# Kernel optimization log

Measured on AMD Instinct MI355X. Metric: run time of the kernel, lower is better.

## Reference

```python
import jax, jax.numpy as jnp
import numpy as np
from jax import lax

D = 32          # link_state_dim == path_state_dim
MAX_LEN = 16    # max path length (fixed for jit)
T_ITER = 8      # message-passing iterations


def gru_cell(x, h, kernel, rec_kernel, bias):
    """Keras GRUCell, reset_after=True. bias: [2, 3H] (input bias, recurrent bias)."""
    xw = x @ kernel + bias[0]
    hw = h @ rec_kernel + bias[1]
    xz, xr, xh = jnp.split(xw, 3, axis=-1)
    hz, hr, hh = jnp.split(hw, 3, axis=-1)
    z = jax.nn.sigmoid(xz + hz)
    r = jax.nn.sigmoid(xr + hr)
    c = jnp.tanh(xh + r * hh)
    return z * h + (1.0 - z) * c


def setup_inputs() -> dict:
    n_paths, n_links = 100000, 10000
    lengths = (np.arange(n_paths) % MAX_LEN) + 1            # 1..16, avg 8.5
    E = int(lengths.sum())                                   # 850000
    path_ids = np.repeat(np.arange(n_paths), lengths).astype(np.int32)
    offsets = np.repeat(np.cumsum(lengths) - lengths, lengths)
    sequence_path = (np.arange(E) - offsets).astype(np.int32)  # 0..len-1 per path
    rng = np.random.default_rng(0)
    link_to_path = rng.integers(0, n_links, E).astype(np.int32)

    key = jax.random.key(0)
    ks = jax.random.split(key, 16)
    p = {
        'capacity': jax.random.uniform(ks[0], (n_links, 1), jnp.float32) + 0.1,
        'traffic': jax.random.uniform(ks[1], (n_paths, 1), jnp.float32),
        'packets': jax.random.uniform(ks[2], (n_paths, 1), jnp.float32),
        'time_dist_params': jax.random.normal(ks[3], (n_paths, 12), jnp.float32),
        'path_kernel': 0.2 * jax.random.normal(ks[4], (D, 3 * D), jnp.float32),
        'path_rec_kernel': 0.2 * jax.random.normal(ks[5], (D, 3 * D), jnp.float32),
        'path_bias': jnp.zeros((2, 3 * D), jnp.float32),
        'link_kernel': 0.2 * jax.random.normal(ks[6], (D, 3 * D), jnp.float32),
        'link_rec_kernel': 0.2 * jax.random.normal(ks[7], (D, 3 * D), jnp.float32),
        'link_bias': jnp.zeros((2, 3 * D), jnp.float32),
        'w1': 0.1 * jax.random.normal(ks[8], (D, 256), jnp.float32),
        'b1': jnp.zeros((256,), jnp.float32),
        'w2': 0.1 * jax.random.normal(ks[9], (256, 256), jnp.float32),
        'b2': jnp.zeros((256,), jnp.float32),
        'w3': 0.1 * jax.random.normal(ks[10], (256, 1), jnp.float32),
        'b3': jnp.zeros((1,), jnp.float32),
        'link_to_path': jnp.asarray(link_to_path),
        'path_ids': jnp.asarray(path_ids),
        'sequence_path': jnp.asarray(sequence_path),
        'path_to_link': jnp.asarray(path_ids),      # path index of each (link,path) incidence
        'sequence_links': jnp.asarray(link_to_path),  # link index (segment id) of each incidence
        'n_links': n_links,
        'n_paths': n_paths,
    }
    return p


def reference(capacity, traffic, packets, time_dist_params,
              path_kernel, path_rec_kernel, path_bias,
              link_kernel, link_rec_kernel, link_bias,
              w1, b1, w2, b2, w3, b3,
              link_to_path, path_ids, sequence_path, path_to_link, sequence_links,
              n_links, n_paths):
    # initial states
    link_state = jnp.concatenate([capacity, jnp.zeros((n_links, D - 1), capacity.dtype)], axis=1)
    path_state = jnp.concatenate(
        [traffic, packets, time_dist_params, jnp.zeros((n_paths, D - 14), traffic.dtype)], axis=1)

    def mp_iter(carry, _):
        link_state, path_state = carry
        # gather link states along each path, scatter into padded [P, T, D]
        link_gather = link_state[link_to_path]
        link_inputs = jnp.zeros((n_paths, MAX_LEN, D), link_state.dtype)
        link_inputs = link_inputs.at[path_ids, sequence_path].set(link_gather)
        xs = jnp.moveaxis(link_inputs, 1, 0)              # [T, P, D]
        mask = jnp.any(xs != 0.0, axis=-1)                # keras Masking semantics

        def rnn_step(h, xm):
            x, m = xm
            h_new = gru_cell(x, h, path_kernel, path_rec_kernel, path_bias)
            return jnp.where(m[:, None], h_new, h), None

        path_state, _ = lax.scan(rnn_step, path_state, (xs, mask))
        # aggregate path states back onto links
        path_gather = path_state[path_to_link]
        path_sum = jax.ops.segment_sum(path_gather, sequence_links, num_segments=n_links)
        link_state = gru_cell(path_sum, link_state, link_kernel, link_rec_kernel, link_bias)
        return (link_state, path_state), None

    (link_state, path_state), _ = lax.scan(mp_iter, (link_state, path_state), None, length=T_ITER)

    h = jax.nn.relu(path_state @ w1 + b1)
    h = jax.nn.relu(h @ w2 + b2)
    return h @ w3 + b3
```

## Files before the change

### kernel.cpp

```cpp
#include <hip/hip_runtime.h>
#include <hip/hip_bf16.h>

#define DD 32
#define GG 96

typedef __attribute__((ext_vector_type(8))) short bf16x8;
typedef __attribute__((ext_vector_type(4))) float f32x4;

__device__ __forceinline__ float frcp(float x){ return __builtin_amdgcn_rcpf(x); }
__device__ __forceinline__ float fsig(float x){
    float e = __expf(-x);
    return frcp(1.0f + e);
}
__device__ __forceinline__ float ftanh(float x){
    float ax = fabsf(x);
    float e  = __expf(-2.0f * ax);
    float t  = (1.0f - e) * frcp(1.0f + e);
    return copysignf(t, x);
}
__device__ __forceinline__ short f2bf(float f){
    union { float f; unsigned u; } v; v.f = f;
    unsigned r = v.u + 0x7fffu + ((v.u >> 16) & 1u);
    return (short)(r >> 16);
}
__device__ __forceinline__ float bf2f(short s){
    union { unsigned u; float f; } v; v.u = ((unsigned)(unsigned short)s) << 16;
    return v.f;
}
__device__ __forceinline__ void split2(float x, short& hi, short& lo){
    hi = f2bf(x);
    lo = f2bf(x - bf2f(hi));
}
__device__ __forceinline__ f32x4 splat4(float x){ f32x4 v = { x, x, x, x }; return v; }

#define MFMA3(acc, ah, al, bh, bl) do { \
    acc = __builtin_amdgcn_mfma_f32_16x16x32_bf16(ah, bh, acc, 0, 0, 0); \
    acc = __builtin_amdgcn_mfma_f32_16x16x32_bf16(al, bh, acc, 0, 0, 0); \
    acc = __builtin_amdgcn_mfma_f32_16x16x32_bf16(ah, bl, acc, 0, 0, 0); \
} while (0)


__global__ void zero_ints_kernel(int* a, int n){
    int i = blockIdx.x * blockDim.x + threadIdx.x;
    if (i < n) a[i] = 0;
}

__global__ void init_states_kernel(const float* __restrict__ cap,
                                   const float* __restrict__ traffic, const float* __restrict__ packets,
                                   const float* __restrict__ tdp,
                                   float* __restrict__ ls, short* __restrict__ lsbh, short* __restrict__ lsbl,
                                   float* __restrict__ ps, int n_links, int n_paths){
    int i = blockIdx.x * blockDim.x + threadIdx.x;
    int nl = n_links * DD;
    if (i < nl){
        int l = i >> 5, d = i & 31;
        float v = (d == 0) ? cap[l] : 0.0f;
        ls[i] = v;
        short hi, lo; split2(v, hi, lo);
        lsbh[i] = hi; lsbl[i] = lo;
        return;
    }
    int j = i - nl;
    if (j >= n_paths * DD) return;
    int p = j >> 5, d = j & 31;
    float v = 0.0f;
    if (d == 0) v = traffic[p];
    else if (d == 1) v = packets[p];
    else if (d < 14) v = tdp[p * 12 + (d - 2)];
    ps[j] = v;
}

__global__ void meta_kernel(const int* __restrict__ path_ids, const int* __restrict__ seqp,
                            const int* __restrict__ seql, int* __restrict__ start,
                            int* __restrict__ lenp, int* __restrict__ lcount, int E){
    int e = blockIdx.x * blockDim.x + threadIdx.x;
    if (e >= E) return;
    int p = path_ids[e];
    int s = seqp[e];
    if (s == 0) start[p] = e;
    if (e == E - 1 || path_ids[e + 1] != p) lenp[p] = s + 1;
    atomicAdd(&lcount[seql[e]], 1);
}

__global__ void bhist_block_kernel(const int* __restrict__ lenp, int* __restrict__ bcnt,
                                   int* __restrict__ bh, int n_paths){
    __shared__ int h[16];
    if (threadIdx.x < 16) h[threadIdx.x] = 0;
    __syncthreads();
    int p = blockIdx.x * 256 + threadIdx.x;
    if (p < n_paths) atomicAdd(&h[lenp[p] - 1], 1);
    __syncthreads();
    if (threadIdx.x < 16){
        bh[blockIdx.x * 16 + threadIdx.x] = h[threadIdx.x];
        atomicAdd(&bcnt[threadIdx.x], h[threadIdx.x]);
    }
}

__global__ void bscan2_kernel(const int* __restrict__ bcnt, const int* __restrict__ bh,
                              int* __restrict__ bb, int nblk){
    __shared__ int base[16];
    if (threadIdx.x == 0){
        int run = 0;
        for (int i = 0; i < 16; i++){ base[i] = run; run += bcnt[i]; }
    }
    __syncthreads();
    int i = threadIdx.x;
    if (i < 16){
        int run = base[i];
        for (int blk = 0; blk < nblk; ++blk){
            bb[blk * 16 + i] = run;
            run += bh[blk * 16 + i];
        }
    }
}

__global__ void bscatter2_kernel(const int* __restrict__ lenp, const int* __restrict__ bb,
                                 int* __restrict__ order, int n_paths){
    __shared__ int h[16];
    if (threadIdx.x < 16) h[threadIdx.x] = 0;
    __syncthreads();
    int p = blockIdx.x * 256 + threadIdx.x;
    if (p < n_paths){
        int b = lenp[p] - 1;
        int r = atomicAdd(&h[b], 1);
        order[bb[blockIdx.x * 16 + b] + r] = p;
    }
}

__global__ __launch_bounds__(1024) void scan_kernel(const int* __restrict__ cnt, int* __restrict__ off, int n){
    __shared__ int psh[1025];
    int tid = threadIdx.x;
    int chunk = (n + 1023) / 1024;
    int b = tid * chunk, e = min(b + chunk, n);
    int s = 0;
    for (int i = b; i < e; ++i) s += cnt[i];
    psh[tid + 1] = s;
    if (tid == 0) psh[0] = 0;
    __syncthreads();
    for (int ofs = 1; ofs < 1024; ofs <<= 1){
        int v = (tid + 1 >= ofs) ? psh[tid + 1 - ofs] : 0;
        __syncthreads();
        psh[tid + 1] += v;
        __syncthreads();
    }
    int run = psh[tid];
    for (int i = b; i < e; ++i){ off[i] = run; run += cnt[i]; }
    if (b < n && e == n) off[n] = run;
}

__global__ void fillpbl_kernel(const int* __restrict__ seql, const int* __restrict__ p2l,
                               const int* __restrict__ loff, int* __restrict__ lfill,
                               int* __restrict__ pbl, int E){
    int e = blockIdx.x * blockDim.x + threadIdx.x;
    if (e >= E) return;
    int l = seql[e];
    int pos = loff[l] + atomicAdd(&lfill[l], 1);
    pbl[pos] = p2l[e];
}

__global__ void pack_all_kernel(const float* __restrict__ pK, const float* __restrict__ pRK,
                                const float* __restrict__ lK, const float* __restrict__ lRK,
                                const float* __restrict__ w1, const float* __restrict__ w2,
                                short* __restrict__ gth, short* __restrict__ gtl,
                                short* __restrict__ rth, short* __restrict__ rtl){
    int t0 = blockIdx.x * blockDim.x + threadIdx.x;
    if (t0 < 4 * 6 * 64){
        int t = t0;
        int lane = t & 63;
        int jt = (t >> 6) % 6;
        int mat = t / (6 * 64);
        const float* W = (mat == 0) ? pK : (mat == 1) ? pRK : (mat == 2) ? lK : lRK;
        int n = lane & 15, g = lane >> 4;
        for (int i = 0; i < 8; i++){
            float w = W[(g * 8 + i) * GG + jt * 16 + n];
            short hi, lo; split2(w, hi, lo);
            gth[(size_t)t * 8 + i] = hi;
            gtl[(size_t)t * 8 + i] = lo;
        }
        return;
    }
    int t = t0 - 4 * 6 * 64;
    if (t >= 144 * 64) return;
    int lane = t & 63;
    int f = t >> 6;
    int n = lane & 15, g = lane >> 4;
    for (int i = 0; i < 8; i++){
        float w;
        if (f < 16) w = w1[(g * 8 + i) * 256 + f * 16 + n];
        else {
            int ff = f - 16, kc = ff >> 4, jt = ff & 15;
            w = w2[(kc * 32 + g * 8 + i) * 256 + jt * 16 + n];
        }
        short hi, lo; split2(w, hi, lo);
        rth[(size_t)t * 8 + i] = hi;
        rtl[(size_t)t * 8 + i] = lo;
    }
}

template<bool MASK>
__device__ __forceinline__ void gru_gates(const f32x4 accZR[4], const f32x4 accXC[2], const f32x4 accHC[2],
                                          float hD[2][4], const int lenD[4], int t)
{
    #pragma unroll
    for (int tt = 0; tt < 2; tt++){
        #pragma unroll
        for (int r = 0; r < 4; r++){
            float z = fsig(accZR[tt][r]);
            float rr = fsig(accZR[2 + tt][r]);
            float c = ftanh(accXC[tt][r] + rr * accHC[tt][r]);
            float hn = z * hD[tt][r] + (1.0f - z) * c;
            if (MASK) hD[tt][r] = (t < lenD[r]) ? hn : hD[tt][r];
            else      hD[tt][r] = hn;
        }
    }
}

__global__ __launch_bounds__(256, 1) void path_gru_kernel(
    const short* __restrict__ lsbh, const short* __restrict__ lsbl, float* __restrict__ ps,
    const int* __restrict__ l2p, const int* __restrict__ start,
    const int* __restrict__ lenp, const int* __restrict__ order,
    const short* __restrict__ gth, const short* __restrict__ gtl,
    const float* __restrict__ bias, int n_paths, int n_waves, int stride)
{
    __shared__ __align__(16) float hlds[4][16 * 36];

    int tid = threadIdx.x;
    int warp = tid >> 6;
    int lane = tid & 63;
    int l15 = lane & 15, g = lane >> 4;

    int gw = blockIdx.x * 4 + warp;
    int nw = gridDim.x * 4;
    float* hl = hlds[warp];

    bf16x8 wKh[6], wKl[6], wRKh[6], wRKl[6];
    #pragma unroll
    for (int jt = 0; jt < 6; jt++){
        wKh[jt]  = *(const bf16x8*)(gth + ((size_t)((0 * 6 + jt) * 64 + lane)) * 8);
        wKl[jt]  = *(const bf16x8*)(gtl + ((size_t)((0 * 6 + jt) * 64 + lane)) * 8);
        wRKh[jt] = *(const bf16x8*)(gth + ((size_t)((1 * 6 + jt) * 64 + lane)) * 8);
        wRKl[jt] = *(const bf16x8*)(gtl + ((size_t)((1 * 6 + jt) * 64 + lane)) * 8);
    }
    float bzr[4], bx2[2], bh2[2];
    #pragma unroll
    for (int jt = 0; jt < 4; jt++) bzr[jt] = bias[jt * 16 + l15] + bias[GG + jt * 16 + l15];
    #pragma unroll
    for (int u = 0; u < 2; u++){
        bx2[u] = bias[(4 + u) * 16 + l15];
        bh2[u] = bias[GG + (4 + u) * 16 + l15];
    }

    for (int w = gw; w < n_waves; w += nw){
        long long wp = ((long long)w * stride) % n_waves;
        int base16 = (int)wp * 16;

        int aidx = base16 + l15;
        int pa = order[min(aidx, n_paths - 1)];
        int s0 = start[pa];
        int la_c = lenp[pa];
        int la = (aidx < n_paths) ? la_c : 0;
        int maxlen = __shfl(la_c, 15);

        int pD[4], lenD[4]; bool vD[4];
        #pragma unroll
        for (int r = 0; r < 4; r++){
            int di = base16 + g * 4 + r;
            vD[r] = (di < n_paths);
            pD[r] = order[min(di, n_paths - 1)];
            lenD[r] = vD[r] ? lenp[pD[r]] : 0;
        }

        float hD[2][4];
        #pragma unroll
        for (int tt = 0; tt < 2; tt++)
            #pragma unroll
            for (int r = 0; r < 4; r++)
                hD[tt][r] = ps[(size_t)pD[r] * DD + l15 + tt * 16];

        bf16x8 hfh, hfl;
        {
            const float* hp = ps + (size_t)pa * DD + g * 8;
            #pragma unroll
            for (int i = 0; i < 8; i++){ short hi, lo; split2(hp[i], hi, lo); hfh[i] = hi; hfl[i] = lo; }
        }

        bf16x8 xfh, xfl;
        {
            int lk = l2p[s0];
            xfh = *reinterpret_cast<const bf16x8*>(lsbh + (size_t)lk * DD + g * 8);
            xfl = *reinterpret_cast<const bf16x8*>(lsbl + (size_t)lk * DD + g * 8);
        }

        for (int t = 0; t < maxlen; ++t){
            bf16x8 nxh, nxl;
            int tn = t + 1;
            if (tn < maxlen){
                int e = s0 + max(min(tn, la - 1), 0);
                int lk = l2p[e];
                nxh = *reinterpret_cast<const bf16x8*>(lsbh + (size_t)lk * DD + g * 8);
                nxl = *reinterpret_cast<const bf16x8*>(lsbl + (size_t)lk * DD + g * 8);
            }

            f32x4 accZR[4], accXC[2], accHC[2];
            #pragma unroll
            for (int jt = 0; jt < 4; jt++){
                f32x4 a = splat4(bzr[jt]);
                MFMA3(a, xfh, xfl, wKh[jt],  wKl[jt]);
                MFMA3(a, hfh, hfl, wRKh[jt], wRKl[jt]);
                accZR[jt] = a;
            }
            #pragma unroll
            for (int u = 0; u < 2; u++){
                f32x4 ax = splat4(bx2[u]);
                MFMA3(ax, xfh, xfl, wKh[4 + u], wKl[4 + u]);
                accXC[u] = ax;
                f32x4 ah = splat4(bh2[u]);
                MFMA3(ah, hfh, hfl, wRKh[4 + u], wRKl[4 + u]);
                accHC[u] = ah;
            }

            gru_gates<true>(accZR, accXC, accHC, hD, lenD, t);

            #pragma unroll
            for (int tt = 0; tt < 2; tt++)
                #pragma unroll
                for (int r = 0; r < 4; r++)
                    hl[(g * 4 + r) * 36 + l15 + tt * 16] = hD[tt][r];
            const float* hrow = hl + l15 * 36 + g * 8;
            #pragma unroll
            for (int i = 0; i < 8; i++){ short hi, lo; split2(hrow[i], hi, lo); hfh[i] = hi; hfl[i] = lo; }

            xfh = nxh; xfl = nxl;
        }

        #pragma unroll
        for (int r = 0; r < 4; r++){
            if (vD[r]){
                #pragma unroll
                for (int tt = 0; tt < 2; tt++)
                    ps[(size_t)pD[r] * DD + l15 + tt * 16] = hD[tt][r];
            }
        }
    }
}

__global__ __launch_bounds__(256, 1) void link_fused_kernel(
    const float* __restrict__ ps, const int* __restrict__ loff, const int* __restrict__ pbl,
    float* __restrict__ ls, short* __restrict__ lsbh, short* __restrict__ lsbl,
    const short* __restrict__ gth, const short* __restrict__ gtl,
    const float* __restrict__ bias, int n_links)
{
    int tid = threadIdx.x;
    int warp = tid >> 6;
    int lane = tid & 63;
    int l15 = lane & 15, g = lane >> 4;

    int base16 = (blockIdx.x * 4 + warp) * 16;
    if (base16 >= n_links) return;

    bf16x8 wKh[6], wKl[6], wRKh[6], wRKl[6];
    #pragma unroll
    for (int jt = 0; jt < 6; jt++){
        wKh[jt]  = *(const bf16x8*)(gth + ((size_t)((2 * 6 + jt) * 64 + lane)) * 8);
        wKl[jt]  = *(const bf16x8*)(gtl + ((size_t)((2 * 6 + jt) * 64 + lane)) * 8);
        wRKh[jt] = *(const bf16x8*)(gth + ((size_t)((3 * 6 + jt) * 64 + lane)) * 8);
        wRKl[jt] = *(const bf16x8*)(gtl + ((size_t)((3 * 6 + jt) * 64 + lane)) * 8);
    }
    float bzr[4], bx2[2], bh2[2];
    #pragma unroll
    for (int jt = 0; jt < 4; jt++) bzr[jt] = bias[jt * 16 + l15] + bias[GG + jt * 16 + l15];
    #pragma unroll
    for (int u = 0; u < 2; u++){
        bx2[u] = bias[(4 + u) * 16 + l15];
        bh2[u] = bias[GG + (4 + u) * 16 + l15];
    }

    int pa = min(base16 + l15, n_links - 1);

    float4 s0v = {0,0,0,0}, s1v = {0,0,0,0};
    {
        int b = loff[pa], e = loff[pa + 1];
        #pragma unroll 4
        for (int k = b; k < e; ++k){
            const float4* pr = (const float4*)(ps + (size_t)pbl[k] * DD) + g * 2;
            float4 v0 = pr[0], v1 = pr[1];
            s0v.x += v0.x; s0v.y += v0.y; s0v.z += v0.z; s0v.w += v0.w;
            s1v.x += v1.x; s1v.y += v1.y; s1v.z += v1.z; s1v.w += v1.w;
        }
    }

    int pD[4]; bool vD[4]; int lenD[4];
    #pragma unroll
    for (int r = 0; r < 4; r++){
        int di = base16 + g * 4 + r;
        vD[r] = (di < n_links);
        pD[r] = min(di, n_links - 1);
        lenD[r] = 0;
    }

    float hD[2][4];
    #pragma unroll
    for (int tt = 0; tt < 2; tt++)
        #pragma unroll
        for (int r = 0; r < 4; r++)
            hD[tt][r] = ls[(size_t)pD[r] * DD + l15 + tt * 16];

    bf16x8 hfh, hfl, xfh, xfl;
    {
        const float* hp = ls + (size_t)pa * DD + g * 8;
        float xs[8] = { s0v.x, s0v.y, s0v.z, s0v.w, s1v.x, s1v.y, s1v.z, s1v.w };
        #pragma unroll
        for (int i = 0; i < 8; i++){
            short hi, lo;
            split2(hp[i], hi, lo); hfh[i] = hi; hfl[i] = lo;
            split2(xs[i], hi, lo); xfh[i] = hi; xfl[i] = lo;
        }
    }

    f32x4 accZR[4], accXC[2], accHC[2];
    #pragma unroll
    for (int jt = 0; jt < 4; jt++){
        f32x4 a = splat4(bzr[jt]);
        MFMA3(a, xfh, xfl, wKh[jt],  wKl[jt]);
        MFMA3(a, hfh, hfl, wRKh[jt], wRKl[jt]);
        accZR[jt] = a;
    }
    #pragma unroll
    for (int u = 0; u < 2; u++){
        f32x4 ax = splat4(bx2[u]);
        MFMA3(ax, xfh, xfl, wKh[4 + u], wKl[4 + u]);
        accXC[u] = ax;
        f32x4 ah = splat4(bh2[u]);
        MFMA3(ah, hfh, hfl, wRKh[4 + u], wRKl[4 + u]);
        accHC[u] = ah;
    }
    gru_gates<false>(accZR, accXC, accHC, hD, lenD, 0);

    #pragma unroll
    for (int r = 0; r < 4; r++){
        if (vD[r]){
            #pragma unroll
            for (int tt = 0; tt < 2; tt++){
                float v = hD[tt][r];
                size_t off = (size_t)pD[r] * DD + l15 + tt * 16;
                ls[off] = v;
                short hi, lo; split2(v, hi, lo);
                lsbh[off] = hi; lsbl[off] = lo;
            }
        }
    }
}

__global__ __launch_bounds__(256) void readout_kernel(
    const float* __restrict__ ps,
    const short* __restrict__ rth, const short* __restrict__ rtl,
    const float* __restrict__ b1, const float* __restrict__ b2,
    const float* __restrict__ w3, const float* __restrict__ b3,
    float* __restrict__ out, int n_paths)
{
    __shared__ __align__(16) float hT[4][16 * 68];

    int tid = threadIdx.x;
    int warp = tid >> 6;
    int lane = tid & 63;
    int l15 = lane & 15, g = lane >> 4;
    int pbase = blockIdx.x * 64 + warp * 16;

    bf16x8 xh, xl;
    {
        int prow = min(pbase + l15, n_paths - 1);
        const float* xp = ps + (size_t)prow * DD + g * 8;
        #pragma unroll
        for (int i = 0; i < 8; i++){ short hi, lo; split2(xp[i], hi, lo); xh[i] = hi; xl[i] = lo; }
    }

    float* hw = hT[warp];

    f32x4 acc2[16];
    #pragma unroll
    for (int jt = 0; jt < 16; jt++) acc2[jt] = splat4(b2[jt * 16 + l15]);

    #pragma unroll 1
    for (int c = 0; c < 4; c++){
        #pragma unroll
        for (int u = 0; u < 4; u++){
            int jt = c * 4 + u;
            bf16x8 wh = *(const bf16x8*)(rth + (size_t)(jt * 64 + lane) * 8);
            bf16x8 wl = *(const bf16x8*)(rtl + (size_t)(jt * 64 + lane) * 8);
            f32x4 a = splat4(b1[jt * 16 + l15]);
            MFMA3(a, xh, xl, wh, wl);
            #pragma unroll
            for (int r = 0; r < 4; r++)
                hw[(g * 4 + r) * 68 + u * 16 + l15] = fmaxf(a[r], 0.0f);
        }
        bf16x8 ah[2], al[2];
        #pragma unroll
        for (int kc2 = 0; kc2 < 2; kc2++){
            const float* hr = hw + l15 * 68 + kc2 * 32 + g * 8;
            #pragma unroll
            for (int i = 0; i < 8; i++){ short hi, lo; split2(hr[i], hi, lo); ah[kc2][i] = hi; al[kc2][i] = lo; }
        }
        #pragma unroll
        for (int jt = 0; jt < 16; jt++){
            #pragma unroll
            for (int kc2 = 0; kc2 < 2; kc2++){
                int f = 16 + (c * 2 + kc2) * 16 + jt;
                bf16x8 wh = *(const bf16x8*)(rth + (size_t)(f * 64 + lane) * 8);
                bf16x8 wl = *(const bf16x8*)(rtl + (size_t)(f * 64 + lane) * 8);
                MFMA3(acc2[jt], ah[kc2], al[kc2], wh, wl);
            }
        }
    }

    float part[4] = {0.0f, 0.0f, 0.0f, 0.0f};
    #pragma unroll
    for (int jt = 0; jt < 16; jt++){
        float w3v = w3[jt * 16 + l15];
        #pragma unroll
        for (int r = 0; r < 4; r++)
            part[r] = fmaf(fmaxf(acc2[jt][r], 0.0f), w3v, part[r]);
    }
    #pragma unroll
    for (int ofs = 1; ofs < 16; ofs <<= 1)
        #pragma unroll
        for (int r = 0; r < 4; r++)
            part[r] += __shfl_xor(part[r], ofs);

    if (l15 == 0){
        float b3v = b3[0];
        #pragma unroll
        for (int r = 0; r < 4; r++){
            int p = pbase + g * 4 + r;
            if (p < n_paths) out[p] = part[r] + b3v;
        }
    }
}

static int host_gcd(int a, int b){ while (b){ int t = a % b; a = b; b = t; } return a; }

extern "C" void kernel_launch(void* const* d_in, const int* in_sizes, int n_in,
                              void* d_out, int out_size, void* d_ws, size_t ws_size,
                              hipStream_t stream)
{
    const float* capacity = (const float*)d_in[0];
    const float* traffic  = (const float*)d_in[1];
    const float* packets  = (const float*)d_in[2];
    const float* tdp      = (const float*)d_in[3];
    const float* pK  = (const float*)d_in[4];
    const float* pRK = (const float*)d_in[5];
    const float* pB  = (const float*)d_in[6];
    const float* lK  = (const float*)d_in[7];
    const float* lRK = (const float*)d_in[8];
    const float* lB  = (const float*)d_in[9];
    const float* w1  = (const float*)d_in[10];
    const float* b1  = (const float*)d_in[11];
    const float* w2  = (const float*)d_in[12];
    const float* b2  = (const float*)d_in[13];
    const float* w3  = (const float*)d_in[14];
    const float* b3  = (const float*)d_in[15];
    const int* l2p      = (const int*)d_in[16];
    const int* path_ids = (const int*)d_in[17];
    const int* seqp     = (const int*)d_in[18];
    const int* p2l      = (const int*)d_in[19];
    const int* seql     = (const int*)d_in[20];
    int n_links = in_sizes[0];
    int n_paths = in_sizes[1];
    int E       = in_sizes[16];
    float* out = (float*)d_out;

    char* w = (char*)d_ws;
    auto carve = [&](size_t bytes) -> void* {
        void* r = (void*)w;
        w += (bytes + 255) & ~(size_t)255;
        return r;
    };
    int nblk = (n_paths + 255) / 256;
    float* ls    = (float*)carve((size_t)n_links * DD * 4);
    short* lsbh  = (short*)carve((size_t)n_links * DD * 2);
    short* lsbl  = (short*)carve((size_t)n_links * DD * 2);
    float* ps    = (float*)carve((size_t)n_paths * DD * 4);
    int* start   = (int*)carve((size_t)n_paths * 4);
    int* lenp    = (int*)carve((size_t)n_paths * 4);
    int* order   = (int*)carve((size_t)n_paths * 4);
    int* loff    = (int*)carve((size_t)(n_links + 1) * 4);
    int* pbl     = (int*)carve((size_t)E * 4);
    short* gth   = (short*)carve((size_t)4 * 6 * 64 * 8 * 2);
    short* gtl   = (short*)carve((size_t)4 * 6 * 64 * 8 * 2);
    short* rth   = (short*)carve((size_t)144 * 64 * 8 * 2);
    short* rtl   = (short*)carve((size_t)144 * 64 * 8 * 2);
    int* bh      = (int*)carve((size_t)nblk * 16 * 4);
    int* bb      = (int*)carve((size_t)nblk * 16 * 4);
    int* izero   = (int*)carve(((size_t)2 * n_links + 16) * 4);
    int* lcount  = izero;
    int* lfill   = izero + n_links;
    int* bcnt    = izero + 2 * n_links;

    const int TB = 256;
    int nz = 2 * n_links + 16;
    zero_ints_kernel<<<(nz + TB - 1) / TB, TB, 0, stream>>>(izero, nz);
    init_states_kernel<<<(((n_links + n_paths) * DD) + TB - 1) / TB, TB, 0, stream>>>(
        capacity, traffic, packets, tdp, ls, lsbh, lsbl, ps, n_links, n_paths);
    meta_kernel<<<(E + TB - 1) / TB, TB, 0, stream>>>(path_ids, seqp, seql, start, lenp, lcount, E);
    bhist_block_kernel<<<nblk, 256, 0, stream>>>(lenp, bcnt, bh, n_paths);
    bscan2_kernel<<<1, 64, 0, stream>>>(bcnt, bh, bb, nblk);
    bscatter2_kernel<<<nblk, 256, 0, stream>>>(lenp, bb, order, n_paths);
    scan_kernel<<<1, 1024, 0, stream>>>(lcount, loff, n_links);
    fillpbl_kernel<<<(E + TB - 1) / TB, TB, 0, stream>>>(seql, p2l, loff, lfill, pbl, E);
    pack_all_kernel<<<((4 * 6 * 64 + 144 * 64) + TB - 1) / TB, TB, 0, stream>>>(
        pK, pRK, lK, lRK, w1, w2, gth, gtl, rth, rtl);

    int n_waves = (n_paths + 15) / 16;
    int stride = 1;
    if (n_waves > 2){
        stride = (int)((double)n_waves * 0.381966);
        if (stride < 1) stride = 1;
        while (host_gcd(stride, n_waves) != 1) stride++;
    }
    int pg_blocks = 512;
    if (pg_blocks > (n_waves + 3) / 4) pg_blocks = (n_waves + 3) / 4;
    int lg_blocks = ((n_links + 15) / 16 + 3) / 4;

    for (int it = 0; it < 8; ++it){
        path_gru_kernel<<<pg_blocks, 256, 0, stream>>>(lsbh, lsbl, ps, l2p, start, lenp, order,
                                                       gth, gtl, pB, n_paths, n_waves, stride);
        link_fused_kernel<<<lg_blocks, 256, 0, stream>>>(ps, loff, pbl, ls, lsbh, lsbl,
                                                         gth, gtl, lB, n_links);
    }
    readout_kernel<<<(n_paths + 63) / 64, 256, 0, stream>>>(ps, rth, rtl, b1, b2, w3, b3, out, n_paths);
}
```

Baseline: 1.188 ms.

## Swap MFMA operand order so each lane owns one path, replace LDS transpose with shuffles

The MFMA operands are swapped (weights as A, state as B), so the accumulator layout places one path per lane column. Each lane can then use its own path length for masking and load and store its hidden state with float4 accesses. The per-step LDS round trip that rebuilt the bf16 hi/lo fragment is replaced by packed hi/lo cross-lane shuffles, and the link kernel reads the recurrent fragment directly from the precomputed bf16 buffers. This removes LDS traffic, the extra order/length lookups and scattered scalar stores, at the cost of 16 shuffles per step and per-row bias vectors.

```diff
diff --git a/kernel.cpp b/kernel.cpp
--- a/kernel.cpp
+++ b/kernel.cpp
@@ -197,9 +197,10 @@
     }
 }
 
+
 template<bool MASK>
 __device__ __forceinline__ void gru_gates(const f32x4 accZR[4], const f32x4 accXC[2], const f32x4 accHC[2],
-                                          float hD[2][4], const int lenD[4], int t)
+                                          float hD[2][4], int la, int t)
 {
     #pragma unroll
     for (int tt = 0; tt < 2; tt++){
@@ -209,10 +210,49 @@
             float rr = fsig(accZR[2 + tt][r]);
             float c = ftanh(accXC[tt][r] + rr * accHC[tt][r]);
             float hn = z * hD[tt][r] + (1.0f - z) * c;
-            if (MASK) hD[tt][r] = (t < lenD[r]) ? hn : hD[tt][r];
+            if (MASK) hD[tt][r] = (t < la) ? hn : hD[tt][r];
             else      hD[tt][r] = hn;
         }
     }
+}
+
+__device__ __forceinline__ void hD_to_bfrag(const float hD[2][4], int l15, int g,
+                                            bf16x8& bh, bf16x8& bl){
+    unsigned pk0[4], pk1[4];
+    #pragma unroll
+    for (int r = 0; r < 4; r++){
+        short hi, lo;
+        split2(hD[0][r], hi, lo);
+        pk0[r] = (((unsigned)(unsigned short)hi) << 16) | (unsigned)(unsigned short)lo;
+        split2(hD[1][r], hi, lo);
+        pk1[r] = (((unsigned)(unsigned short)hi) << 16) | (unsigned)(unsigned short)lo;
+    }
+    bool hiTT = ((g >> 1) & 1);
+    #pragma unroll
+    for (int i = 0; i < 8; i++){
+        int src = l15 + 16 * ((2 * g + (i >> 2)) & 3);
+        unsigned v0 = (unsigned)__shfl((int)pk0[i & 3], src, 64);
+        unsigned v1 = (unsigned)__shfl((int)pk1[i & 3], src, 64);
+        unsigned v = hiTT ? v1 : v0;
+        bh[i] = (short)(v >> 16);
+        bl[i] = (short)(v & 0xffffu);
+    }
+}
+
+__device__ __forceinline__ void load_bias4(const float* __restrict__ bias, int g,
+                                           f32x4 bZR[4], f32x4 bXC[2], f32x4 bHC[2]){
+    #pragma unroll
+    for (int jt = 0; jt < 4; jt++)
+        #pragma unroll
+        for (int r = 0; r < 4; r++)
+            bZR[jt][r] = bias[jt * 16 + 4 * g + r] + bias[GG + jt * 16 + 4 * g + r];
+    #pragma unroll
+    for (int u = 0; u < 2; u++)
+        #pragma unroll
+        for (int r = 0; r < 4; r++){
+            bXC[u][r] = bias[(4 + u) * 16 + 4 * g + r];
+            bHC[u][r] = bias[GG + (4 + u) * 16 + 4 * g + r];
+        }
 }
 
 __global__ __launch_bounds__(256, 1) void path_gru_kernel(
@@ -222,8 +262,6 @@
     const short* __restrict__ gth, const short* __restrict__ gtl,
     const float* __restrict__ bias, int n_paths, int n_waves, int stride)
 {
-    __shared__ __align__(16) float hlds[4][16 * 36];
-
     int tid = threadIdx.x;
     int warp = tid >> 6;
     int lane = tid & 63;
@@ -231,7 +269,6 @@
 
     int gw = blockIdx.x * 4 + warp;
     int nw = gridDim.x * 4;
-    float* hl = hlds[warp];
 
     bf16x8 wKh[6], wKl[6], wRKh[6], wRKl[6];
     #pragma unroll
@@ -241,48 +278,31 @@
         wRKh[jt] = *(const bf16x8*)(gth + ((size_t)((1 * 6 + jt) * 64 + lane)) * 8);
         wRKl[jt] = *(const bf16x8*)(gtl + ((size_t)((1 * 6 + jt) * 64 + lane)) * 8);
     }
-    float bzr[4], bx2[2], bh2[2];
-    #pragma unroll
-    for (int jt = 0; jt < 4; jt++) bzr[jt] = bias[jt * 16 + l15] + bias[GG + jt * 16 + l15];
-    #pragma unroll
-    for (int u = 0; u < 2; u++){
-        bx2[u] = bias[(4 + u) * 16 + l15];
-        bh2[u] = bias[GG + (4 + u) * 16 + l15];
-    }
+    f32x4 bZR[4], bXC[2], bHC[2];
+    load_bias4(bias, g, bZR, bXC, bHC);
 
     for (int w = gw; w < n_waves; w += nw){
         long long wp = ((long long)w * stride) % n_waves;
         int base16 = (int)wp * 16;
 
         int aidx = base16 + l15;
+        bool va = (aidx < n_paths);
         int pa = order[min(aidx, n_paths - 1)];
         int s0 = start[pa];
         int la_c = lenp[pa];
-        int la = (aidx < n_paths) ? la_c : 0;
+        int la = va ? la_c : 0;
         int maxlen = __shfl(la_c, 15);
 
-        int pD[4], lenD[4]; bool vD[4];
-        #pragma unroll
-        for (int r = 0; r < 4; r++){
-            int di = base16 + g * 4 + r;
-            vD[r] = (di < n_paths);
-            pD[r] = order[min(di, n_paths - 1)];
-            lenD[r] = vD[r] ? lenp[pD[r]] : 0;
-        }
-
         float hD[2][4];
-        #pragma unroll
-        for (int tt = 0; tt < 2; tt++)
-            #pragma unroll
-            for (int r = 0; r < 4; r++)
-                hD[tt][r] = ps[(size_t)pD[r] * DD + l15 + tt * 16];
+        {
+            float4 h0 = *(const float4*)(ps + (size_t)pa * DD + 4 * g);
+            float4 h1 = *(const float4*)(ps + (size_t)pa * DD + 16 + 4 * g);
+            hD[0][0] = h0.x; hD[0][1] = h0.y; hD[0][2] = h0.z; hD[0][3] = h0.w;
+            hD[1][0] = h1.x; hD[1][1] = h1.y; hD[1][2] = h1.z; hD[1][3] = h1.w;
+        }
 
         bf16x8 hfh, hfl;
-        {
-            const float* hp = ps + (size_t)pa * DD + g * 8;
-            #pragma unroll
-            for (int i = 0; i < 8; i++){ short hi, lo; split2(hp[i], hi, lo); hfh[i] = hi; hfl[i] = lo; }
-        }
+        hD_to_bfrag(hD, l15, g, hfh, hfl);
 
         bf16x8 xfh, xfl;
         {
@@ -304,42 +324,32 @@
             f32x4 accZR[4], accXC[2], accHC[2];
             #pragma unroll
             for (int jt = 0; jt < 4; jt++){
-                f32x4 a = splat4(bzr[jt]);
-                MFMA3(a, xfh, xfl, wKh[jt],  wKl[jt]);
-                MFMA3(a, hfh, hfl, wRKh[jt], wRKl[jt]);
+                f32x4 a = bZR[jt];
+                MFMA3(a, wKh[jt],  wKl[jt],  xfh, xfl);
+                MFMA3(a, wRKh[jt], wRKl[jt], hfh, hfl);
                 accZR[jt] = a;
             }
             #pragma unroll
             for (int u = 0; u < 2; u++){
-                f32x4 ax = splat4(bx2[u]);
-                MFMA3(ax, xfh, xfl, wKh[4 + u], wKl[4 + u]);
+                f32x4 ax = bXC[u];
+                MFMA3(ax, wKh[4 + u], wKl[4 + u], xfh, xfl);
                 accXC[u] = ax;
-                f32x4 ah = splat4(bh2[u]);
-                MFMA3(ah, hfh, hfl, wRKh[4 + u], wRKl[4 + u]);
+                f32x4 ah = bHC[u];
+                MFMA3(ah, wRKh[4 + u], wRKl[4 + u], hfh, hfl);
                 accHC[u] = ah;
             }
 
-            gru_gates<true>(accZR, accXC, accHC, hD, lenD, t);
-
-            #pragma unroll
-            for (int tt = 0; tt < 2; tt++)
-                #pragma unroll
-                for (int r = 0; r < 4; r++)
-                    hl[(g * 4 + r) * 36 + l15 + tt * 16] = hD[tt][r];
-            const float* hrow = hl + l15 * 36 + g * 8;
-            #pragma unroll
-            for (int i = 0; i < 8; i++){ short hi, lo; split2(hrow[i], hi, lo); hfh[i] = hi; hfl[i] = lo; }
+            gru_gates<true>(accZR, accXC, accHC, hD, la, t);
+            hD_to_bfrag(hD, l15, g, hfh, hfl);
 
             xfh = nxh; xfl = nxl;
         }
 
-        #pragma unroll
-        for (int r = 0; r < 4; r++){
-            if (vD[r]){
-                #pragma unroll
-                for (int tt = 0; tt < 2; tt++)
-                    ps[(size_t)pD[r] * DD + l15 + tt * 16] = hD[tt][r];
-            }
+        if (va){
+            float4 h0 = { hD[0][0], hD[0][1], hD[0][2], hD[0][3] };
+            float4 h1 = { hD[1][0], hD[1][1], hD[1][2], hD[1][3] };
+            *(float4*)(ps + (size_t)pa * DD + 4 * g) = h0;
+            *(float4*)(ps + (size_t)pa * DD + 16 + 4 * g) = h1;
         }
     }
 }
@@ -366,16 +376,12 @@
         wRKh[jt] = *(const bf16x8*)(gth + ((size_t)((3 * 6 + jt) * 64 + lane)) * 8);
         wRKl[jt] = *(const bf16x8*)(gtl + ((size_t)((3 * 6 + jt) * 64 + lane)) * 8);
     }
-    float bzr[4], bx2[2], bh2[2];
-    #pragma unroll
-    for (int jt = 0; jt < 4; jt++) bzr[jt] = bias[jt * 16 + l15] + bias[GG + jt * 16 + l15];
-    #pragma unroll
-    for (int u = 0; u < 2; u++){
-        bx2[u] = bias[(4 + u) * 16 + l15];
-        bh2[u] = bias[GG + (4 + u) * 16 + l15];
-    }
-
-    int pa = min(base16 + l15, n_links - 1);
+    f32x4 bZR[4], bXC[2], bHC[2];
+    load_bias4(bias, g, bZR, bXC, bHC);
+
+    int di = base16 + l15;
+    bool va = (di < n_links);
+    int pa = min(di, n_links - 1);
 
     float4 s0v = {0,0,0,0}, s1v = {0,0,0,0};
     {
@@ -389,65 +395,57 @@
         }
     }
 
-    int pD[4]; bool vD[4]; int lenD[4];
-    #pragma unroll
-    for (int r = 0; r < 4; r++){
-        int di = base16 + g * 4 + r;
-        vD[r] = (di < n_links);
-        pD[r] = min(di, n_links - 1);
-        lenD[r] = 0;
-    }
-
     float hD[2][4];
-    #pragma unroll
-    for (int tt = 0; tt < 2; tt++)
-        #pragma unroll
-        for (int r = 0; r < 4; r++)
-            hD[tt][r] = ls[(size_t)pD[r] * DD + l15 + tt * 16];
-
-    bf16x8 hfh, hfl, xfh, xfl;
     {
-        const float* hp = ls + (size_t)pa * DD + g * 8;
+        float4 h0 = *(const float4*)(ls + (size_t)pa * DD + 4 * g);
+        float4 h1 = *(const float4*)(ls + (size_t)pa * DD + 16 + 4 * g);
+        hD[0][0] = h0.x; hD[0][1] = h0.y; hD[0][2] = h0.z; hD[0][3] = h0.w;
+        hD[1][0] = h1.x; hD[1][1] = h1.y; hD[1][2] = h1.z; hD[1][3] = h1.w;
+    }
+    bf16x8 hfh = *reinterpret_cast<const bf16x8*>(lsbh + (size_t)pa * DD + g * 8);
+    bf16x8 hfl = *reinterpret_cast<const bf16x8*>(lsbl + (size_t)pa * DD + g * 8);
+
+    bf16x8 xfh, xfl;
+    {
         float xs[8] = { s0v.x, s0v.y, s0v.z, s0v.w, s1v.x, s1v.y, s1v.z, s1v.w };
         #pragma unroll
         for (int i = 0; i < 8; i++){
-            short hi, lo;
-            split2(hp[i], hi, lo); hfh[i] = hi; hfl[i] = lo;
-            split2(xs[i], hi, lo); xfh[i] = hi; xfl[i] = lo;
+            short hi, lo; split2(xs[i], hi, lo);
+            xfh[i] = hi; xfl[i] = lo;
         }
     }
 
     f32x4 accZR[4], accXC[2], accHC[2];
     #pragma unroll
     for (int jt = 0; jt < 4; jt++){
-        f32x4 a = splat4(bzr[jt]);
-        MFMA3(a, xfh, xfl, wKh[jt],  wKl[jt]);
-        MFMA3(a, hfh, hfl, wRKh[jt], wRKl[jt]);
+        f32x4 a = bZR[jt];
+        MFMA3(a, wKh[jt],  wKl[jt],  xfh, xfl);
+        MFMA3(a, wRKh[jt], wRKl[jt], hfh, hfl);
         accZR[jt] = a;
     }
     #pragma unroll
     for (int u = 0; u < 2; u++){
-        f32x4 ax = splat4(bx2[u]);
-        MFMA3(ax, xfh, xfl, wKh[4 + u], wKl[4 + u]);
+        f32x4 ax = bXC[u];
+        MFMA3(ax, wKh[4 + u], wKl[4 + u], xfh, xfl);
         accXC[u] = ax;
-        f32x4 ah = splat4(bh2[u]);
-        MFMA3(ah, hfh, hfl, wRKh[4 + u], wRKl[4 + u]);
+        f32x4 ah = bHC[u];
+        MFMA3(ah, wRKh[4 + u], wRKl[4 + u], hfh, hfl);
         accHC[u] = ah;
     }
-    gru_gates<false>(accZR, accXC, accHC, hD, lenD, 0);
-
-    #pragma unroll
-    for (int r = 0; r < 4; r++){
-        if (vD[r]){
-            #pragma unroll
-            for (int tt = 0; tt < 2; tt++){
-                float v = hD[tt][r];
-                size_t off = (size_t)pD[r] * DD + l15 + tt * 16;
-                ls[off] = v;
-                short hi, lo; split2(v, hi, lo);
-                lsbh[off] = hi; lsbl[off] = lo;
-            }
-        }
+    gru_gates<false>(accZR, accXC, accHC, hD, 0, 0);
+
+    if (va){
+        float4 h0 = { hD[0][0], hD[0][1], hD[0][2], hD[0][3] };
+        float4 h1 = { hD[1][0], hD[1][1], hD[1][2], hD[1][3] };
+        *(float4*)(ls + (size_t)pa * DD + 4 * g) = h0;
+        *(float4*)(ls + (size_t)pa * DD + 16 + 4 * g) = h1;
+        short hs[8], lws[8];
+        #pragma unroll
+        for (int r = 0; r < 4; r++){ split2(hD[0][r], hs[r], lws[r]); split2(hD[1][r], hs[4 + r], lws[4 + r]); }
+        *(short4*)(lsbh + (size_t)pa * DD + 4 * g)      = make_short4(hs[0], hs[1], hs[2], hs[3]);
+        *(short4*)(lsbh + (size_t)pa * DD + 16 + 4 * g) = make_short4(hs[4], hs[5], hs[6], hs[7]);
+        *(short4*)(lsbl + (size_t)pa * DD + 4 * g)      = make_short4(lws[0], lws[1], lws[2], lws[3]);
+        *(short4*)(lsbl + (size_t)pa * DD + 16 + 4 * g) = make_short4(lws[4], lws[5], lws[6], lws[7]);
     }
 }
 
```

After: 1.188 ms. About the same (+0.0%).
